# Performance work log

Measured on AMD Instinct MI355X. Metric: run time of the kernel, lower is better.

Reference implementation:

```python
import jax, jax.numpy as jnp
import numpy as np

N = 170000      # nodes
E = 2400000     # edges
F_IN = 128      # dataset.num_features
H = 64          # hidden_channels
C = 40          # dataset.num_classes
L = 8           # num_layers
ENTROPY = 1.0   # args.entropy
EPS = 1e-20


def setup_inputs() -> dict:
    key = jax.random.key(0)
    ks = jax.random.split(key, 10)
    x = jax.random.normal(ks[0], (N, F_IN), jnp.float32)
    edge_src = jax.random.randint(ks[1], (E,), 0, N)
    edge_dst = jax.random.randint(ks[2], (E,), 0, N)
    edge_weight = jax.random.uniform(ks[3], (E,), jnp.float32) / 14.0  # ~1/deg scale
    u = jax.random.uniform(ks[4], (N, L + 1), jnp.float32, 1e-6, 1.0 - 1e-6)
    gumbel = -jnp.log(-jnp.log(u))  # standard Gumbel noise for gumbel_softmax
    lin0_w = jax.random.normal(ks[5], (F_IN, H), jnp.float32) / np.float32(np.sqrt(F_IN))
    lin0_b = jnp.zeros((H,), jnp.float32)
    meta_w = jax.random.normal(ks[6], (H, 1), jnp.float32) / np.float32(np.sqrt(H))
    meta_b = jnp.zeros((1,), jnp.float32)
    lin1_w = jax.random.normal(ks[7], (H, C), jnp.float32) / np.float32(np.sqrt(H))
    lin1_b = jnp.zeros((C,), jnp.float32)
    return dict(x=x, edge_weight=edge_weight, gumbel=gumbel,
                lin0_w=lin0_w, lin0_b=lin0_b, meta_w=meta_w, meta_b=meta_b,
                lin1_w=lin1_w, lin1_b=lin1_b,
                edge_src=edge_src, edge_dst=edge_dst)


def reference(x, edge_weight, gumbel, lin0_w, lin0_b, meta_w, meta_b,
              lin1_w, lin1_b, edge_src, edge_dst):
    # input projection + relu (dropout=0 -> no-op)
    x = jnp.maximum(x @ lin0_w + lin0_b, 0.0)  # [N,H]
    xs = [x]
    # GCNII layers with conv.alpha = conv.beta = 0 -> pure edge-weighted
    # scatter-add propagation followed by relu.
    for _ in range(L):
        msg = edge_weight[:, None] * x[edge_src]              # [E,H] gather
        x = jax.ops.segment_sum(msg, edge_dst, num_segments=N)  # [N,H] scatter-add
        x = jnp.maximum(x, 0.0)
        xs.append(x)
    xMat = jnp.stack(xs, axis=1)  # [N, L+1, H] (preds == xMatrix since concat='none')
    # MetaNet: [N, L+1]
    r = jnp.squeeze(xMat @ meta_w, -1) + meta_b[0]
    # get_t: stick-breaking with sigmoid; last column uses t=1 times cumprod
    s = jax.nn.sigmoid(r)                                    # [N, L+1]
    cp_excl = jnp.concatenate(
        [jnp.ones((N, 1), s.dtype), jnp.cumprod(1.0 - s, axis=1)[:, :-1]], axis=1)
    t = s * cp_excl
    t = t.at[:, -1].set(cp_excl[:, -1])
    ent_loss = ENTROPY * (-(jnp.log(t + EPS) * t).sum(1).mean())
    # gumbel_softmax(log(t+eps), tau=1, hard=False)
    tM = jax.nn.softmax(jnp.log(t + EPS) + gumbel, axis=1)   # [N, L+1]
    # layer mixing: [N,1,L+1] @ [N,L+1,H] -> [N,H]
    out = jnp.einsum('nl,nlh->nh', tM, xMat)
    out = out @ lin1_w + lin1_b
    return jax.nn.log_softmax(out, axis=-1), ent_loss
```

## Files before the change

kernel.cpp:

```cpp
#include <hip/hip_runtime.h>
#include <hip/hip_bf16.h>

#define N_NODES 170000
#define N_EDGES 2400000
#define F_IN_   128
#define H_      64
#define C_OUT   40
#define L_LAYERS 8
#define LP1     9
#define EPS_T   1e-20f
#define ROW_ELEMS (LP1 * H_)

typedef unsigned short u16;
typedef unsigned short u16x8 __attribute__((ext_vector_type(8)));
typedef short bf16x8 __attribute__((ext_vector_type(8)));
typedef float f32x4 __attribute__((ext_vector_type(4)));

__device__ __forceinline__ float bf2f(u16 u) {
    union { unsigned int i; float f; } c; c.i = ((unsigned int)u) << 16; return c.f;
}
__device__ __forceinline__ u16 f2bf(float f) {
    __hip_bfloat16 h = __float2bfloat16(f);
    return *reinterpret_cast<u16*>(&h);
}

__device__ __forceinline__ float waveReduceSum(float v) {
    for (int m = 32; m; m >>= 1) v += __shfl_xor(v, m, 64);
    return v;
}

__global__ __launch_bounds__(256) void k_zero4(float4* __restrict__ p) {
    p[blockIdx.x * 256 + threadIdx.x] = make_float4(0.f, 0.f, 0.f, 0.f);
}

__global__ __launch_bounds__(256) void k_hist(
    const int* __restrict__ edst, int* __restrict__ deg)
{
    int e = blockIdx.x * 256 + threadIdx.x;
    if (e < N_EDGES) atomicAdd(&deg[edst[e]], 1);
}

#define SCAN_TPB 256
#define SCAN_VPT 8
#define SCAN_EPB (SCAN_TPB * SCAN_VPT)
#define SCAN_BLOCKS ((N_NODES + SCAN_EPB - 1) / SCAN_EPB)

__global__ __launch_bounds__(SCAN_TPB) void k_scan1(
    const int* __restrict__ deg, int* __restrict__ rowstart,
    int* __restrict__ blockSums)
{
    __shared__ int tsum[SCAN_TPB];
    int tid = threadIdx.x;
    int base = blockIdx.x * SCAN_EPB + tid * SCAN_VPT;
    int vals[SCAN_VPT];
    int local = 0;
    #pragma unroll
    for (int i = 0; i < SCAN_VPT; ++i) {
        int idx = base + i;
        int v = (idx < N_NODES) ? deg[idx] : 0;
        vals[i] = local;
        local += v;
    }
    tsum[tid] = local;
    __syncthreads();
    for (int off = 1; off < SCAN_TPB; off <<= 1) {
        int v = (tid >= off) ? tsum[tid - off] : 0;
        __syncthreads();
        tsum[tid] += v;
        __syncthreads();
    }
    int texcl = tsum[tid] - local;
    #pragma unroll
    for (int i = 0; i < SCAN_VPT; ++i) {
        int idx = base + i;
        if (idx < N_NODES) rowstart[idx] = texcl + vals[i];
    }
    if (tid == SCAN_TPB - 1) blockSums[blockIdx.x] = tsum[tid];
}

__global__ __launch_bounds__(64) void k_scan2(int* __restrict__ blockSums) {
    if (threadIdx.x == 0) {
        int acc = 0;
        for (int i = 0; i < SCAN_BLOCKS; ++i) {
            int v = blockSums[i];
            blockSums[i] = acc;
            acc += v;
        }
    }
}

__global__ __launch_bounds__(SCAN_TPB) void k_scan3(
    int* __restrict__ rowstart, const int* __restrict__ blockSums)
{
    int off = blockSums[blockIdx.x];
    int base = blockIdx.x * SCAN_EPB + threadIdx.x * SCAN_VPT;
    #pragma unroll
    for (int i = 0; i < SCAN_VPT; ++i) {
        int idx = base + i;
        if (idx < N_NODES) rowstart[idx] += off;
    }
}

__global__ __launch_bounds__(256) void k_bucket(
    const int* __restrict__ esrc, const int* __restrict__ edst,
    const float* __restrict__ ew, const int* __restrict__ rowstart,
    int* __restrict__ cursor, int2* __restrict__ csr, int lo, int hi)
{
    int e = blockIdx.x * 256 + threadIdx.x;
    if (e >= N_EDGES) return;
    int d = edst[e];
    if (d < lo || d >= hi) return;
    int p = rowstart[d] + atomicAdd(&cursor[d], 1);
    csr[p] = make_int2(esrc[e], __float_as_int(ew[e]));
}

__global__ __launch_bounds__(256) void k_lin0(
    const float* __restrict__ x, const float* __restrict__ W0,
    const float* __restrict__ b0, const float* __restrict__ mw,
    const float* __restrict__ mb, u16* __restrict__ xMatB,
    float* __restrict__ r)
{
    __shared__ u16 Wt[H_ * F_IN_];
    int tid = threadIdx.x;
    for (int i = tid; i < F_IN_ * H_; i += 256) {
        int k = i >> 6, c = i & 63;
        Wt[c * F_IN_ + (k ^ ((c & 7) << 3))] = f2bf(W0[i]);
    }
    __syncthreads();

    int wave = tid >> 6, lane = tid & 63;
    int lg = lane >> 4;
    int lr = lane & 15;

    bf16x8 bfrag[4][4];
    float b0v[4], mwv[4];
    #pragma unroll
    for (int ct = 0; ct < 4; ++ct) {
        int c = ct * 16 + lr;
        #pragma unroll
        for (int kt = 0; kt < 4; ++kt) {
            int kidx = (kt * 32 + lg * 8) ^ ((c & 7) << 3);
            bfrag[ct][kt] = *reinterpret_cast<bf16x8*>(&Wt[c * F_IN_ + kidx]);
        }
        b0v[ct] = b0[c];
        mwv[ct] = mw[c];
    }
    float mb0 = mb[0];

    int nbase = blockIdx.x * 256 + wave * 64;
    #pragma unroll
    for (int m = 0; m < 4; ++m) {
        int arow = nbase + m * 16 + lr;
        int arowc = (arow < N_NODES) ? arow : (N_NODES - 1);
        const float4* xrow = (const float4*)(x + (size_t)arowc * F_IN_);
        f32x4 acc[4];
        #pragma unroll
        for (int ct = 0; ct < 4; ++ct) {
            acc[ct][0] = b0v[ct]; acc[ct][1] = b0v[ct];
            acc[ct][2] = b0v[ct]; acc[ct][3] = b0v[ct];
        }
        #pragma unroll
        for (int kt = 0; kt < 4; ++kt) {
            int k8 = kt * 8 + lg * 2;
            float4 xa = xrow[k8];
            float4 xb = xrow[k8 + 1];
            bf16x8 a;
            a[0] = (short)f2bf(xa.x); a[1] = (short)f2bf(xa.y);
            a[2] = (short)f2bf(xa.z); a[3] = (short)f2bf(xa.w);
            a[4] = (short)f2bf(xb.x); a[5] = (short)f2bf(xb.y);
            a[6] = (short)f2bf(xb.z); a[7] = (short)f2bf(xb.w);
            #pragma unroll
            for (int ct = 0; ct < 4; ++ct)
                acc[ct] = __builtin_amdgcn_mfma_f32_16x16x32_bf16(
                    a, bfrag[ct][kt], acc[ct], 0, 0, 0);
        }
        float p[4];
        #pragma unroll
        for (int reg = 0; reg < 4; ++reg) {
            int n = nbase + m * 16 + lg * 4 + reg;
            float pr = 0.f;
            #pragma unroll
            for (int ct = 0; ct < 4; ++ct) {
                float v = fmaxf(acc[ct][reg], 0.f);
                if (n < N_NODES)
                    xMatB[(size_t)n * ROW_ELEMS + ct * 16 + lr] = f2bf(v);
                pr = fmaf(v, mwv[ct], pr);
            }
            p[reg] = pr;
        }
        #pragma unroll
        for (int reg = 0; reg < 4; ++reg) {
            p[reg] += __shfl_xor(p[reg], 1, 64);
            p[reg] += __shfl_xor(p[reg], 2, 64);
            p[reg] += __shfl_xor(p[reg], 4, 64);
            p[reg] += __shfl_xor(p[reg], 8, 64);
        }
        if (lr < 4) {
            int n = nbase + m * 16 + lg * 4 + lr;
            if (n < N_NODES) r[n * LP1] = p[lr] + mb0;
        }
    }
}

__global__ __launch_bounds__(256) void k_prop(
    const u16* __restrict__ xMatB, int l,
    const int* __restrict__ rowstart, const int* __restrict__ deg,
    const int2* __restrict__ csr,
    const float* __restrict__ mw, const float* __restrict__ mb,
    u16* __restrict__ xMatOut, float* __restrict__ r)
{
    int tid = threadIdx.x;
    int oc = tid & 7;
    int n = blockIdx.x * 32 + (tid >> 3);
    bool valid = (n < N_NODES);
    int start = valid ? rowstart[n] : 0;
    int d     = valid ? deg[n]      : 0;

    const unsigned loff = (unsigned)l * H_ + oc * 8;
    float acc0[8] = {0.f,0.f,0.f,0.f,0.f,0.f,0.f,0.f};
    float acc1[8] = {0.f,0.f,0.f,0.f,0.f,0.f,0.f,0.f};

    int t = 0;
    while (__any(t < d)) {
        if (t < d) {
            int2 e = csr[start + t];
            float w = __int_as_float(e.y);
            u16x8 v = *reinterpret_cast<const u16x8*>(
                &xMatB[(size_t)(unsigned)e.x * ROW_ELEMS + loff]);
            #pragma unroll
            for (int j = 0; j < 8; ++j) acc0[j] = fmaf(bf2f(v[j]), w, acc0[j]);
        }
        if (t + 1 < d) {
            int2 e = csr[start + t + 1];
            float w = __int_as_float(e.y);
            u16x8 v = *reinterpret_cast<const u16x8*>(
                &xMatB[(size_t)(unsigned)e.x * ROW_ELEMS + loff]);
            #pragma unroll
            for (int j = 0; j < 8; ++j) acc1[j] = fmaf(bf2f(v[j]), w, acc1[j]);
        }
        t += 2;
    }

    float a[8];
    #pragma unroll
    for (int j = 0; j < 8; ++j) a[j] = fmaxf(acc0[j] + acc1[j], 0.f);

    if (valid) {
        u16x8 o;
        #pragma unroll
        for (int j = 0; j < 8; ++j) o[j] = f2bf(a[j]);
        *reinterpret_cast<u16x8*>(
            &xMatOut[(size_t)n * ROW_ELEMS + (l + 1) * H_ + oc * 8]) = o;
    }
    float dot = 0.f;
    #pragma unroll
    for (int j = 0; j < 8; ++j) dot = fmaf(a[j], mw[oc * 8 + j], dot);
    dot += __shfl_xor(dot, 1, 64);
    dot += __shfl_xor(dot, 2, 64);
    dot += __shfl_xor(dot, 4, 64);
    if (valid && oc == 0) r[n * LP1 + (l + 1)] = dot + mb[0];
}

__global__ __launch_bounds__(256) void k_gate(
    const float* __restrict__ r, const float* __restrict__ gum,
    float* __restrict__ tM, float* __restrict__ entPart)
{
    __shared__ float lds[4];
    int tid = threadIdx.x;
    int n = blockIdx.x * 256 + tid;
    float ent = 0.f;
    if (n < N_NODES) {
        float t[LP1], lg[LP1];
        float cp = 1.f;
        #pragma unroll
        for (int j = 0; j < LP1; ++j) {
            float rv = r[n * LP1 + j];
            float s = 1.f / (1.f + expf(-rv));
            t[j] = (j == L_LAYERS) ? cp : s * cp;
            cp *= (1.f - s);
        }
        float mx = -INFINITY;
        #pragma unroll
        for (int j = 0; j < LP1; ++j) {
            float lt = logf(t[j] + EPS_T);
            ent -= t[j] * lt;
            lg[j] = lt + gum[n * LP1 + j];
            mx = fmaxf(mx, lg[j]);
        }
        float se = 0.f;
        #pragma unroll
        for (int j = 0; j < LP1; ++j) { lg[j] = expf(lg[j] - mx); se += lg[j]; }
        float inv = 1.f / se;
        #pragma unroll
        for (int j = 0; j < LP1; ++j) tM[n * LP1 + j] = lg[j] * inv;
    }
    float s = waveReduceSum(ent);
    int wave = tid >> 6, lane = tid & 63;
    if (lane == 0) lds[wave] = s;
    __syncthreads();
    if (tid == 0) entPart[blockIdx.x] = lds[0] + lds[1] + lds[2] + lds[3];
}

__global__ __launch_bounds__(256) void k_mix(
    const u16* __restrict__ xMatB, const float* __restrict__ tM,
    u16* __restrict__ mix)
{
    int t = blockIdx.x * 256 + threadIdx.x;
    int n = t >> 3, oc = t & 7;
    if (n >= N_NODES) return;
    const u16* row = &xMatB[(size_t)n * ROW_ELEMS + oc * 8];
    const float* tMn = &tM[n * LP1];
    float acc[8] = {0.f,0.f,0.f,0.f,0.f,0.f,0.f,0.f};
    #pragma unroll
    for (int j = 0; j < LP1; ++j) {
        u16x8 v = *reinterpret_cast<const u16x8*>(&row[j * H_]);
        float w = tMn[j];
        #pragma unroll
        for (int q = 0; q < 8; ++q) acc[q] = fmaf(bf2f(v[q]), w, acc[q]);
    }
    u16x8 o;
    #pragma unroll
    for (int q = 0; q < 8; ++q) o[q] = f2bf(acc[q]);
    *reinterpret_cast<u16x8*>(&mix[(size_t)n * H_ + oc * 8]) = o;
}

__global__ __launch_bounds__(256) void k_lin1(
    const u16* __restrict__ mix, const float* __restrict__ W1,
    const float* __restrict__ b1, float* __restrict__ out)
{
    __shared__ u16 Wl[48 * 64];
    int tid = threadIdx.x;
    for (int i = tid; i < 48 * 64; i += 256) {
        int c = i >> 6, k = i & 63;
        float v = (c < C_OUT) ? W1[k * C_OUT + c] : 0.f;
        Wl[c * 64 + (k ^ ((c & 7) << 3))] = f2bf(v);
    }
    __syncthreads();

    int wave = tid >> 6, lane = tid & 63;
    int lg = lane >> 4, lr = lane & 15;

    bf16x8 bfrag[3][2];
    float b1v[3];
    #pragma unroll
    for (int ct = 0; ct < 3; ++ct) {
        int c = ct * 16 + lr;
        #pragma unroll
        for (int kt = 0; kt < 2; ++kt) {
            int kidx = (kt * 32 + lg * 8) ^ ((c & 7) << 3);
            bfrag[ct][kt] = *reinterpret_cast<bf16x8*>(&Wl[c * 64 + kidx]);
        }
        b1v[ct] = (c < C_OUT) ? b1[c] : 0.f;
    }

    int nbase = blockIdx.x * 64 + wave * 16;
    int arow = nbase + lr;
    int arowc = (arow < N_NODES) ? arow : (N_NODES - 1);
    const u16* mrow = &mix[(size_t)arowc * H_];

    f32x4 acc[3];
    #pragma unroll
    for (int ct = 0; ct < 3; ++ct) {
        acc[ct][0] = b1v[ct]; acc[ct][1] = b1v[ct];
        acc[ct][2] = b1v[ct]; acc[ct][3] = b1v[ct];
    }
    #pragma unroll
    for (int kt = 0; kt < 2; ++kt) {
        bf16x8 a = *reinterpret_cast<const bf16x8*>(&mrow[kt * 32 + lg * 8]);
        #pragma unroll
        for (int ct = 0; ct < 3; ++ct)
            acc[ct] = __builtin_amdgcn_mfma_f32_16x16x32_bf16(
                a, bfrag[ct][kt], acc[ct], 0, 0, 0);
    }
    #pragma unroll
    for (int reg = 0; reg < 4; ++reg) {
        float v0 = acc[0][reg], v1 = acc[1][reg];
        float v2 = (lr < 8) ? acc[2][reg] : -INFINITY;
        float mx = fmaxf(fmaxf(v0, v1), v2);
        mx = fmaxf(mx, __shfl_xor(mx, 1, 64));
        mx = fmaxf(mx, __shfl_xor(mx, 2, 64));
        mx = fmaxf(mx, __shfl_xor(mx, 4, 64));
        mx = fmaxf(mx, __shfl_xor(mx, 8, 64));
        float e = expf(v0 - mx) + expf(v1 - mx) + ((lr < 8) ? expf(v2 - mx) : 0.f);
        e += __shfl_xor(e, 1, 64);
        e += __shfl_xor(e, 2, 64);
        e += __shfl_xor(e, 4, 64);
        e += __shfl_xor(e, 8, 64);
        float ls = mx + logf(e);
        int n = nbase + lg * 4 + reg;
        if (n < N_NODES) {
            out[(size_t)n * C_OUT + lr]      = v0 - ls;
            out[(size_t)n * C_OUT + 16 + lr] = v1 - ls;
            if (lr < 8) out[(size_t)n * C_OUT + 32 + lr] = v2 - ls;
        }
    }
}

__global__ __launch_bounds__(256) void k_entreduce(
    const float* __restrict__ part, int n, float scale, float* __restrict__ out)
{
    __shared__ float lds[4];
    int tid = threadIdx.x;
    float s = 0.f;
    for (int i = tid; i < n; i += 256) s += part[i];
    s = waveReduceSum(s);
    int wave = tid >> 6, lane = tid & 63;
    if (lane == 0) lds[wave] = s;
    __syncthreads();
    if (tid == 0) out[0] = (lds[0] + lds[1] + lds[2] + lds[3]) * scale;
}

extern "C" void kernel_launch(void* const* d_in, const int* in_sizes, int n_in,
                              void* d_out, int out_size, void* d_ws, size_t ws_size,
                              hipStream_t stream)
{
    const float* x   = (const float*)d_in[0];
    const float* ew  = (const float*)d_in[1];
    const float* gum = (const float*)d_in[2];
    const float* W0  = (const float*)d_in[3];
    const float* b0  = (const float*)d_in[4];
    const float* mw  = (const float*)d_in[5];
    const float* mb  = (const float*)d_in[6];
    const float* W1  = (const float*)d_in[7];
    const float* b1  = (const float*)d_in[8];
    const int* esrc  = (const int*)d_in[9];
    const int* edst  = (const int*)d_in[10];
    float* out = (float*)d_out;

    const size_t xMatBytes = (size_t)N_NODES * ROW_ELEMS * sizeof(u16);
    const size_t tMBytes   = (size_t)N_NODES * LP1 * sizeof(float);
    const size_t entBytes  = (size_t)((N_NODES + 255) / 256) * sizeof(float);
    const size_t rBytes    = (size_t)N_NODES * LP1 * sizeof(float);
    const size_t degBytes  = (size_t)N_NODES * sizeof(int);
    const size_t curBytes  = (size_t)N_NODES * sizeof(int);
    const size_t rowBytes  = (size_t)N_NODES * sizeof(int);
    const size_t bsBytes   = 512;
    const size_t csrBytes  = (size_t)N_EDGES * sizeof(int2);
    const size_t mixBytes  = (size_t)N_NODES * H_ * sizeof(u16);
    const size_t need = xMatBytes + tMBytes + entBytes + rBytes + degBytes +
                        curBytes + rowBytes + bsBytes + csrBytes;
    if (ws_size < need) return;

    char* p = (char*)d_ws;
    u16*  xMatB    = (u16*)p;           p += xMatBytes;
    float* tMbuf   = (float*)p;         p += tMBytes;
    float* entP    = (float*)p;         p += entBytes;
    char* overlay  = p;
    float* rbuf    = (float*)p;         p += rBytes;
    int*  deg      = (int*)p;           p += degBytes;
    int*  cursor   = (int*)p;           p += curBytes;
    int*  rowstart = (int*)p;           p += rowBytes;
    int*  blockSums= (int*)p;           p += bsBytes;
    int2* csr      = (int2*)p;
    u16*  mixbuf   = (u16*)overlay;

    const int edgeBlocks = (N_EDGES + 255) / 256;
    const int gateBlocks = (N_NODES + 255) / 256;
    const int lin0Blocks = (N_NODES + 255) / 256;
    const int propBlocks = (N_NODES + 31) / 32;
    const int mixBlocks  = (N_NODES * 8 + 255) / 256;
    const int lin1Blocks = (N_NODES + 63) / 64;

    k_zero4<<<333, 256, 0, stream>>>((float4*)deg);
    k_hist<<<edgeBlocks, 256, 0, stream>>>(edst, deg);
    k_scan1<<<SCAN_BLOCKS, SCAN_TPB, 0, stream>>>(deg, rowstart, blockSums);
    k_scan2<<<1, 64, 0, stream>>>(blockSums);
    k_scan3<<<SCAN_BLOCKS, SCAN_TPB, 0, stream>>>(rowstart, blockSums);
    const int STEP = N_NODES / 8;
    for (int i = 0; i < 8; ++i)
        k_bucket<<<edgeBlocks, 256, 0, stream>>>(esrc, edst, ew, rowstart,
                                                 cursor, csr, i * STEP,
                                                 (i + 1) * STEP);

    k_lin0<<<lin0Blocks, 256, 0, stream>>>(x, W0, b0, mw, mb, xMatB, rbuf);
    for (int l = 0; l < L_LAYERS; ++l)
        k_prop<<<propBlocks, 256, 0, stream>>>(xMatB, l, rowstart, deg, csr,
                                               mw, mb, xMatB, rbuf);
    k_gate<<<gateBlocks, 256, 0, stream>>>(rbuf, gum, tMbuf, entP);
    k_mix<<<mixBlocks, 256, 0, stream>>>(xMatB, tMbuf, mixbuf);
    k_lin1<<<lin1Blocks, 256, 0, stream>>>(mixbuf, W1, b1, out);
    k_entreduce<<<1, 256, 0, stream>>>(entP, gateBlocks, 1.0f / N_NODES,
                                       out + (size_t)N_NODES * C_OUT);
}
```

Before: 841.5 us.

## Replace global-atomic degree histogram with windowed LDS histogram and merge

Computes node in-degrees with 32 blocks that each scan all edges six times, accumulating packed 16-bit counters in shared memory per node window. A merge kernel then sums the per-block partials into deg. This aims to remove contention from global atomics. The prop kernel's output store becomes nontemporal. The trade-off is repeated full reads of the edge array by only a few blocks, plus extra workspace for the partial histograms.

```diff
diff --git a/kernel.cpp b/kernel.cpp
--- a/kernel.cpp
+++ b/kernel.cpp
@@ -12,6 +12,7 @@
 #define ROW_ELEMS (LP1 * H_)
 
 typedef unsigned short u16;
+typedef unsigned int u32;
 typedef unsigned short u16x8 __attribute__((ext_vector_type(8)));
 typedef short bf16x8 __attribute__((ext_vector_type(8)));
 typedef float f32x4 __attribute__((ext_vector_type(4)));
@@ -33,11 +34,51 @@
     p[blockIdx.x * 256 + threadIdx.x] = make_float4(0.f, 0.f, 0.f, 0.f);
 }
 
-__global__ __launch_bounds__(256) void k_hist(
-    const int* __restrict__ edst, int* __restrict__ deg)
-{
-    int e = blockIdx.x * 256 + threadIdx.x;
-    if (e < N_EDGES) atomicAdd(&deg[edst[e]], 1);
+#define HB 32
+#define HW 32768
+#define HWORDS 16384
+#define HWIN 6
+
+__global__ __launch_bounds__(256) void k_hist2(
+    const int4* __restrict__ edst4, u32* __restrict__ partial)
+{
+    __shared__ u32 h[HWORDS];
+    int b = blockIdx.x, tid = threadIdx.x;
+    for (int w = 0; w < HWIN; ++w) {
+        for (int i = tid; i < HWORDS; i += 256) h[i] = 0;
+        __syncthreads();
+        int lo = w * HW, hi = lo + HW;
+        for (int t = b * 256 + tid; t < N_EDGES / 4; t += HB * 256) {
+            int4 d = edst4[t];
+            int dx;
+            dx = d.x - lo; if ((unsigned)dx < (unsigned)HW)
+                atomicAdd(&h[dx >> 1], 1u << ((dx & 1) << 4));
+            dx = d.y - lo; if ((unsigned)dx < (unsigned)HW)
+                atomicAdd(&h[dx >> 1], 1u << ((dx & 1) << 4));
+            dx = d.z - lo; if ((unsigned)dx < (unsigned)HW)
+                atomicAdd(&h[dx >> 1], 1u << ((dx & 1) << 4));
+            dx = d.w - lo; if ((unsigned)dx < (unsigned)HW)
+                atomicAdd(&h[dx >> 1], 1u << ((dx & 1) << 4));
+        }
+        __syncthreads();
+        u32* dst = &partial[((size_t)w * HB + b) * HWORDS];
+        for (int i = tid; i < HWORDS; i += 256) dst[i] = h[i];
+        __syncthreads();
+    }
+}
+
+__global__ __launch_bounds__(256) void k_histmerge(
+    const u32* __restrict__ partial, int* __restrict__ deg)
+{
+    int gw = blockIdx.x * 256 + threadIdx.x;
+    if (gw >= HWIN * HWORDS) return;
+    int win = gw / HWORDS, word = gw - win * HWORDS;
+    u32 s = 0;
+    for (int b = 0; b < HB; ++b)
+        s += partial[((size_t)win * HB + b) * HWORDS + word];
+    int n0 = win * HW + word * 2;
+    if (n0 < N_NODES)     deg[n0]     = (int)(s & 0xffffu);
+    if (n0 + 1 < N_NODES) deg[n0 + 1] = (int)(s >> 16);
 }
 
 #define SCAN_TPB 256
@@ -249,8 +290,8 @@
         u16x8 o;
         #pragma unroll
         for (int j = 0; j < 8; ++j) o[j] = f2bf(a[j]);
-        *reinterpret_cast<u16x8*>(
-            &xMatOut[(size_t)n * ROW_ELEMS + (l + 1) * H_ + oc * 8]) = o;
+        __builtin_nontemporal_store(o, reinterpret_cast<u16x8*>(
+            &xMatOut[(size_t)n * ROW_ELEMS + (l + 1) * H_ + oc * 8]));
     }
     float dot = 0.f;
     #pragma unroll
@@ -436,9 +477,10 @@
     const size_t rowBytes  = (size_t)N_NODES * sizeof(int);
     const size_t bsBytes   = 512;
     const size_t csrBytes  = (size_t)N_EDGES * sizeof(int2);
+    const size_t partBytes = (size_t)HWIN * HB * HWORDS * sizeof(u32);
     const size_t mixBytes  = (size_t)N_NODES * H_ * sizeof(u16);
     const size_t need = xMatBytes + tMBytes + entBytes + rBytes + degBytes +
-                        curBytes + rowBytes + bsBytes + csrBytes;
+                        curBytes + rowBytes + bsBytes + csrBytes + partBytes;
     if (ws_size < need) return;
 
     char* p = (char*)d_ws;
@@ -451,7 +493,8 @@
     int*  cursor   = (int*)p;           p += curBytes;
     int*  rowstart = (int*)p;           p += rowBytes;
     int*  blockSums= (int*)p;           p += bsBytes;
-    int2* csr      = (int2*)p;
+    int2* csr      = (int2*)p;          p += csrBytes;
+    u32*  partials = (u32*)p;
     u16*  mixbuf   = (u16*)overlay;
 
     const int edgeBlocks = (N_EDGES + 255) / 256;
@@ -460,9 +503,11 @@
     const int propBlocks = (N_NODES + 31) / 32;
     const int mixBlocks  = (N_NODES * 8 + 255) / 256;
     const int lin1Blocks = (N_NODES + 63) / 64;
-
-    k_zero4<<<333, 256, 0, stream>>>((float4*)deg);
-    k_hist<<<edgeBlocks, 256, 0, stream>>>(edst, deg);
+    const int mergeBlocks = (HWIN * HWORDS + 255) / 256;
+
+    k_zero4<<<167, 256, 0, stream>>>((float4*)cursor);
+    k_hist2<<<HB, 256, 0, stream>>>((const int4*)edst, partials);
+    k_histmerge<<<mergeBlocks, 256, 0, stream>>>(partials, deg);
     k_scan1<<<SCAN_BLOCKS, SCAN_TPB, 0, stream>>>(deg, rowstart, blockSums);
     k_scan2<<<1, 64, 0, stream>>>(blockSums);
     k_scan3<<<SCAN_BLOCKS, SCAN_TPB, 0, stream>>>(rowstart, blockSums);
```

Result: slower. 895.6 us (+6.4%).

## Fuse gate and mix kernels, move meta dot out of prop, split histogram

Applied to the files above, without the earlier changes.

Removes the per-layer meta-score dot product and r writes from lin0 and prop, and recomputes the scores in a new fused gate+mix kernel. That kernel reads each node's 9 layer rows once, computes the gumbel-softmax weights in registers and writes the mixed features, so the r and tM buffers and one kernel launch go away. The degree histogram is split into four range-filtered launches to localize the atomics, and prop's output stores become nontemporal. In exchange the edge list is read four times in the histogram, and the layout no longer overlays the mix buffer on the CSR region.

```diff
diff --git a/kernel.cpp b/kernel.cpp
--- a/kernel.cpp
+++ b/kernel.cpp
@@ -12,6 +12,7 @@
 #define ROW_ELEMS (LP1 * H_)
 
 typedef unsigned short u16;
+typedef unsigned int u32;
 typedef unsigned short u16x8 __attribute__((ext_vector_type(8)));
 typedef short bf16x8 __attribute__((ext_vector_type(8)));
 typedef float f32x4 __attribute__((ext_vector_type(4)));
@@ -34,10 +35,13 @@
 }
 
 __global__ __launch_bounds__(256) void k_hist(
-    const int* __restrict__ edst, int* __restrict__ deg)
+    const int* __restrict__ edst, int* __restrict__ deg, int lo, int hi)
 {
     int e = blockIdx.x * 256 + threadIdx.x;
-    if (e < N_EDGES) atomicAdd(&deg[edst[e]], 1);
+    if (e >= N_EDGES) return;
+    int d = edst[e];
+    if (d < lo || d >= hi) return;
+    atomicAdd(&deg[d], 1);
 }
 
 #define SCAN_TPB 256
@@ -116,9 +120,7 @@
 
 __global__ __launch_bounds__(256) void k_lin0(
     const float* __restrict__ x, const float* __restrict__ W0,
-    const float* __restrict__ b0, const float* __restrict__ mw,
-    const float* __restrict__ mb, u16* __restrict__ xMatB,
-    float* __restrict__ r)
+    const float* __restrict__ b0, u16* __restrict__ xMatB)
 {
     __shared__ u16 Wt[H_ * F_IN_];
     int tid = threadIdx.x;
@@ -133,7 +135,7 @@
     int lr = lane & 15;
 
     bf16x8 bfrag[4][4];
-    float b0v[4], mwv[4];
+    float b0v[4];
     #pragma unroll
     for (int ct = 0; ct < 4; ++ct) {
         int c = ct * 16 + lr;
@@ -143,9 +145,7 @@
             bfrag[ct][kt] = *reinterpret_cast<bf16x8*>(&Wt[c * F_IN_ + kidx]);
         }
         b0v[ct] = b0[c];
-        mwv[ct] = mw[c];
-    }
-    float mb0 = mb[0];
+    }
 
     int nbase = blockIdx.x * 256 + wave * 64;
     #pragma unroll
@@ -174,30 +174,16 @@
                 acc[ct] = __builtin_amdgcn_mfma_f32_16x16x32_bf16(
                     a, bfrag[ct][kt], acc[ct], 0, 0, 0);
         }
-        float p[4];
         #pragma unroll
         for (int reg = 0; reg < 4; ++reg) {
             int n = nbase + m * 16 + lg * 4 + reg;
-            float pr = 0.f;
-            #pragma unroll
-            for (int ct = 0; ct < 4; ++ct) {
-                float v = fmaxf(acc[ct][reg], 0.f);
-                if (n < N_NODES)
+            if (n < N_NODES) {
+                #pragma unroll
+                for (int ct = 0; ct < 4; ++ct) {
+                    float v = fmaxf(acc[ct][reg], 0.f);
                     xMatB[(size_t)n * ROW_ELEMS + ct * 16 + lr] = f2bf(v);
-                pr = fmaf(v, mwv[ct], pr);
+                }
             }
-            p[reg] = pr;
-        }
-        #pragma unroll
-        for (int reg = 0; reg < 4; ++reg) {
-            p[reg] += __shfl_xor(p[reg], 1, 64);
-            p[reg] += __shfl_xor(p[reg], 2, 64);
-            p[reg] += __shfl_xor(p[reg], 4, 64);
-            p[reg] += __shfl_xor(p[reg], 8, 64);
-        }
-        if (lr < 4) {
-            int n = nbase + m * 16 + lg * 4 + lr;
-            if (n < N_NODES) r[n * LP1] = p[lr] + mb0;
         }
     }
 }
@@ -205,9 +191,7 @@
 __global__ __launch_bounds__(256) void k_prop(
     const u16* __restrict__ xMatB, int l,
     const int* __restrict__ rowstart, const int* __restrict__ deg,
-    const int2* __restrict__ csr,
-    const float* __restrict__ mw, const float* __restrict__ mb,
-    u16* __restrict__ xMatOut, float* __restrict__ r)
+    const int2* __restrict__ csr, u16* __restrict__ xMatOut)
 {
     int tid = threadIdx.x;
     int oc = tid & 7;
@@ -241,87 +225,93 @@
         t += 2;
     }
 
-    float a[8];
-    #pragma unroll
-    for (int j = 0; j < 8; ++j) a[j] = fmaxf(acc0[j] + acc1[j], 0.f);
-
     if (valid) {
         u16x8 o;
         #pragma unroll
-        for (int j = 0; j < 8; ++j) o[j] = f2bf(a[j]);
-        *reinterpret_cast<u16x8*>(
-            &xMatOut[(size_t)n * ROW_ELEMS + (l + 1) * H_ + oc * 8]) = o;
-    }
-    float dot = 0.f;
-    #pragma unroll
-    for (int j = 0; j < 8; ++j) dot = fmaf(a[j], mw[oc * 8 + j], dot);
-    dot += __shfl_xor(dot, 1, 64);
-    dot += __shfl_xor(dot, 2, 64);
-    dot += __shfl_xor(dot, 4, 64);
-    if (valid && oc == 0) r[n * LP1 + (l + 1)] = dot + mb[0];
-}
-
-__global__ __launch_bounds__(256) void k_gate(
-    const float* __restrict__ r, const float* __restrict__ gum,
-    float* __restrict__ tM, float* __restrict__ entPart)
+        for (int j = 0; j < 8; ++j) o[j] = f2bf(fmaxf(acc0[j] + acc1[j], 0.f));
+        __builtin_nontemporal_store(o, reinterpret_cast<u16x8*>(
+            &xMatOut[(size_t)n * ROW_ELEMS + (l + 1) * H_ + oc * 8]));
+    }
+}
+
+__global__ __launch_bounds__(256) void k_gatemix(
+    const u16* __restrict__ xMatB, const float* __restrict__ gum,
+    const float* __restrict__ mw, const float* __restrict__ mb,
+    u16* __restrict__ mix, float* __restrict__ entPart)
 {
     __shared__ float lds[4];
     int tid = threadIdx.x;
-    int n = blockIdx.x * 256 + tid;
-    float ent = 0.f;
-    if (n < N_NODES) {
-        float t[LP1], lg[LP1];
-        float cp = 1.f;
-        #pragma unroll
-        for (int j = 0; j < LP1; ++j) {
-            float rv = r[n * LP1 + j];
-            float s = 1.f / (1.f + expf(-rv));
-            t[j] = (j == L_LAYERS) ? cp : s * cp;
-            cp *= (1.f - s);
-        }
-        float mx = -INFINITY;
-        #pragma unroll
-        for (int j = 0; j < LP1; ++j) {
-            float lt = logf(t[j] + EPS_T);
-            ent -= t[j] * lt;
-            lg[j] = lt + gum[n * LP1 + j];
-            mx = fmaxf(mx, lg[j]);
-        }
-        float se = 0.f;
-        #pragma unroll
-        for (int j = 0; j < LP1; ++j) { lg[j] = expf(lg[j] - mx); se += lg[j]; }
-        float inv = 1.f / se;
-        #pragma unroll
-        for (int j = 0; j < LP1; ++j) tM[n * LP1 + j] = lg[j] * inv;
-    }
-    float s = waveReduceSum(ent);
+    int oc = tid & 7;
+    int n = blockIdx.x * 32 + (tid >> 3);
+    bool valid = (n < N_NODES);
+    int nc = valid ? n : (N_NODES - 1);
+    const u16* row = &xMatB[(size_t)nc * ROW_ELEMS + oc * 8];
+
+    float mwv[8];
+    #pragma unroll
+    for (int q = 0; q < 8; ++q) mwv[q] = mw[oc * 8 + q];
+    float mb0 = mb[0];
+
+    u16x8 v[LP1];
+    float r[LP1];
+    #pragma unroll
+    for (int j = 0; j < LP1; ++j) {
+        v[j] = *reinterpret_cast<const u16x8*>(&row[j * H_]);
+        float dot = 0.f;
+        #pragma unroll
+        for (int q = 0; q < 8; ++q) dot = fmaf(bf2f(v[j][q]), mwv[q], dot);
+        dot += __shfl_xor(dot, 1, 64);
+        dot += __shfl_xor(dot, 2, 64);
+        dot += __shfl_xor(dot, 4, 64);
+        r[j] = dot + mb0;
+    }
+    float gmine = valid ? gum[(size_t)n * LP1 + oc] : 0.f;
+    float g8    = (valid && oc == 0) ? gum[(size_t)n * LP1 + 8] : 0.f;
+    int gbase = tid & 56;
+
+    float t[LP1], lg[LP1];
+    float cp = 1.f;
+    #pragma unroll
+    for (int j = 0; j < LP1; ++j) {
+        float s = 1.f / (1.f + expf(-r[j]));
+        t[j] = (j == L_LAYERS) ? cp : s * cp;
+        cp *= (1.f - s);
+    }
+    float ent = 0.f, mx = -INFINITY;
+    #pragma unroll
+    for (int j = 0; j < LP1; ++j) {
+        float lt = logf(t[j] + EPS_T);
+        ent -= t[j] * lt;
+        float g = (j < 8) ? __shfl(gmine, (gbase & 56) + j, 64)
+                          : __shfl(g8, gbase & 56, 64);
+        lg[j] = lt + g;
+        mx = fmaxf(mx, lg[j]);
+    }
+    float se = 0.f;
+    #pragma unroll
+    for (int j = 0; j < LP1; ++j) { lg[j] = expf(lg[j] - mx); se += lg[j]; }
+    float inv = 1.f / se;
+
+    float acc[8] = {0.f,0.f,0.f,0.f,0.f,0.f,0.f,0.f};
+    #pragma unroll
+    for (int j = 0; j < LP1; ++j) {
+        float w = lg[j] * inv;
+        #pragma unroll
+        for (int q = 0; q < 8; ++q) acc[q] = fmaf(bf2f(v[j][q]), w, acc[q]);
+    }
+    if (valid) {
+        u16x8 o;
+        #pragma unroll
+        for (int q = 0; q < 8; ++q) o[q] = f2bf(acc[q]);
+        *reinterpret_cast<u16x8*>(&mix[(size_t)n * H_ + oc * 8]) = o;
+    }
+
+    float e = (valid && oc == 0) ? ent : 0.f;
+    e = waveReduceSum(e);
     int wave = tid >> 6, lane = tid & 63;
-    if (lane == 0) lds[wave] = s;
+    if (lane == 0) lds[wave] = e;
     __syncthreads();
     if (tid == 0) entPart[blockIdx.x] = lds[0] + lds[1] + lds[2] + lds[3];
-}
-
-__global__ __launch_bounds__(256) void k_mix(
-    const u16* __restrict__ xMatB, const float* __restrict__ tM,
-    u16* __restrict__ mix)
-{
-    int t = blockIdx.x * 256 + threadIdx.x;
-    int n = t >> 3, oc = t & 7;
-    if (n >= N_NODES) return;
-    const u16* row = &xMatB[(size_t)n * ROW_ELEMS + oc * 8];
-    const float* tMn = &tM[n * LP1];
-    float acc[8] = {0.f,0.f,0.f,0.f,0.f,0.f,0.f,0.f};
-    #pragma unroll
-    for (int j = 0; j < LP1; ++j) {
-        u16x8 v = *reinterpret_cast<const u16x8*>(&row[j * H_]);
-        float w = tMn[j];
-        #pragma unroll
-        for (int q = 0; q < 8; ++q) acc[q] = fmaf(bf2f(v[q]), w, acc[q]);
-    }
-    u16x8 o;
-    #pragma unroll
-    for (int q = 0; q < 8; ++q) o[q] = f2bf(acc[q]);
-    *reinterpret_cast<u16x8*>(&mix[(size_t)n * H_ + oc * 8]) = o;
 }
 
 __global__ __launch_bounds__(256) void k_lin1(
@@ -427,58 +417,55 @@
     const int* edst  = (const int*)d_in[10];
     float* out = (float*)d_out;
 
+    const int propBlocks = (N_NODES + 31) / 32;
+
     const size_t xMatBytes = (size_t)N_NODES * ROW_ELEMS * sizeof(u16);
-    const size_t tMBytes   = (size_t)N_NODES * LP1 * sizeof(float);
-    const size_t entBytes  = (size_t)((N_NODES + 255) / 256) * sizeof(float);
-    const size_t rBytes    = (size_t)N_NODES * LP1 * sizeof(float);
     const size_t degBytes  = (size_t)N_NODES * sizeof(int);
     const size_t curBytes  = (size_t)N_NODES * sizeof(int);
     const size_t rowBytes  = (size_t)N_NODES * sizeof(int);
     const size_t bsBytes   = 512;
     const size_t csrBytes  = (size_t)N_EDGES * sizeof(int2);
     const size_t mixBytes  = (size_t)N_NODES * H_ * sizeof(u16);
-    const size_t need = xMatBytes + tMBytes + entBytes + rBytes + degBytes +
-                        curBytes + rowBytes + bsBytes + csrBytes;
+    const size_t entBytes  = (size_t)propBlocks * sizeof(float);
+    const size_t need = xMatBytes + degBytes + curBytes + rowBytes + bsBytes +
+                        csrBytes + mixBytes + entBytes;
     if (ws_size < need) return;
 
     char* p = (char*)d_ws;
     u16*  xMatB    = (u16*)p;           p += xMatBytes;
-    float* tMbuf   = (float*)p;         p += tMBytes;
-    float* entP    = (float*)p;         p += entBytes;
-    char* overlay  = p;
-    float* rbuf    = (float*)p;         p += rBytes;
     int*  deg      = (int*)p;           p += degBytes;
     int*  cursor   = (int*)p;           p += curBytes;
     int*  rowstart = (int*)p;           p += rowBytes;
     int*  blockSums= (int*)p;           p += bsBytes;
-    int2* csr      = (int2*)p;
-    u16*  mixbuf   = (u16*)overlay;
+    int2* csr      = (int2*)p;          p += csrBytes;
+    u16*  mixbuf   = (u16*)p;           p += mixBytes;
+    float* entP    = (float*)p;
 
     const int edgeBlocks = (N_EDGES + 255) / 256;
-    const int gateBlocks = (N_NODES + 255) / 256;
     const int lin0Blocks = (N_NODES + 255) / 256;
-    const int propBlocks = (N_NODES + 31) / 32;
-    const int mixBlocks  = (N_NODES * 8 + 255) / 256;
+    const int gmixBlocks = propBlocks;
     const int lin1Blocks = (N_NODES + 63) / 64;
 
     k_zero4<<<333, 256, 0, stream>>>((float4*)deg);
-    k_hist<<<edgeBlocks, 256, 0, stream>>>(edst, deg);
+    const int STEP_H = N_NODES / 4;
+    for (int i = 0; i < 4; ++i)
+        k_hist<<<edgeBlocks, 256, 0, stream>>>(edst, deg, i * STEP_H,
+                                               (i + 1) * STEP_H);
     k_scan1<<<SCAN_BLOCKS, SCAN_TPB, 0, stream>>>(deg, rowstart, blockSums);
     k_scan2<<<1, 64, 0, stream>>>(blockSums);
     k_scan3<<<SCAN_BLOCKS, SCAN_TPB, 0, stream>>>(rowstart, blockSums);
-    const int STEP = N_NODES / 8;
+    const int STEP_B = N_NODES / 8;
     for (int i = 0; i < 8; ++i)
         k_bucket<<<edgeBlocks, 256, 0, stream>>>(esrc, edst, ew, rowstart,
-                                                 cursor, csr, i * STEP,
-                                                 (i + 1) * STEP);
-
-    k_lin0<<<lin0Blocks, 256, 0, stream>>>(x, W0, b0, mw, mb, xMatB, rbuf);
+                                                 cursor, csr, i * STEP_B,
+                                                 (i + 1) * STEP_B);
+
+    k_lin0<<<lin0Blocks, 256, 0, stream>>>(x, W0, b0, xMatB);
     for (int l = 0; l < L_LAYERS; ++l)
         k_prop<<<propBlocks, 256, 0, stream>>>(xMatB, l, rowstart, deg, csr,
-                                               mw, mb, xMatB, rbuf);
-    k_gate<<<gateBlocks, 256, 0, stream>>>(rbuf, gum, tMbuf, entP);
-    k_mix<<<mixBlocks, 256, 0, stream>>>(xMatB, tMbuf, mixbuf);
+                                               xMatB);
+    k_gatemix<<<gmixBlocks, 256, 0, stream>>>(xMatB, gum, mw, mb, mixbuf, entP);
     k_lin1<<<lin1Blocks, 256, 0, stream>>>(mixbuf, W1, b1, out);
-    k_entreduce<<<1, 256, 0, stream>>>(entP, gateBlocks, 1.0f / N_NODES,
+    k_entreduce<<<1, 256, 0, stream>>>(entP, gmixBlocks, 1.0f / N_NODES,
                                        out + (size_t)N_NODES * C_OUT);
 }
```

New measurement: 839.9 us. About the same (-0.2%).
